# Performance work log

Measured on AMD Instinct MI355X. Metric: run time of the kernel, lower is better.

## Reference

```python
import jax, jax.numpy as jnp
import numpy as np

HID = 64
CTX = 64
STEPS = 2
RANK = 16
NODES = 1024
B, T = 16, 24
EPS = 1e-5


def _linear(x, W, b):
    # torch nn.Linear: x @ W.T + b, W is [out, in]
    return jnp.einsum('...i,oi->...o', x, W) + b


def _gelu(x):
    return jax.nn.gelu(x, approximate=False)


def _diffusion(adj, state, Ws, bs):
    # Ws: [S, out, in], bs: [S, out]
    term = jnp.zeros_like(state)
    for s in range(Ws.shape[0]):
        state = jnp.einsum('nm,btmf->btnf', adj, state)
        term = term + _linear(state, Ws[s], bs[s])
    return term


def setup_inputs() -> dict:
    key = jax.random.key(0)
    ks = jax.random.split(key, 32)
    f32 = jnp.float32
    def w(k, *shape, scale=None):
        s = scale if scale is not None else 1.0 / np.sqrt(shape[-1])
        return jax.random.uniform(k, shape, f32, -s, s)
    inp = {
        'x': jax.random.normal(ks[0], (B, T, NODES, HID), f32),
        'a_fwd': jax.random.uniform(ks[1], (NODES, NODES), f32),
        'context': jax.random.normal(ks[2], (B, T, NODES, CTX), f32),
        'W_self': w(ks[3], HID, HID), 'b_self': w(ks[4], HID),
        'W_fwd': w(ks[5], STEPS, HID, HID), 'b_fwd': w(ks[6], STEPS, HID),
        'W_bwd': w(ks[7], STEPS, HID, HID), 'b_bwd': w(ks[8], STEPS, HID),
        'W_adp': w(ks[9], STEPS, HID, HID), 'b_adp': w(ks[10], STEPS, HID),
        'Wg1': w(ks[11], HID, CTX), 'bg1': w(ks[12], HID),
        'Wg2': w(ks[13], 4, HID), 'bg2': w(ks[14], 4),
        'Ws1': w(ks[15], HID, CTX), 'bs1': w(ks[16], HID),
        'Ws2': w(ks[17], HID, HID), 'bs2': w(ks[18], HID),
        'W_src': w(ks[19], 1, CTX), 'b_src': w(ks[20], 1),
        'W_dst': w(ks[21], 1, CTX), 'b_dst': w(ks[22], 1),
        'emb_src': jax.random.normal(ks[23], (NODES, RANK), f32) * 0.02,
        'emb_dst': jax.random.normal(ks[24], (NODES, RANK), f32) * 0.02,
        'gamma': jnp.ones((HID,), f32), 'beta': jnp.zeros((HID,), f32),
    }
    return inp


def reference(x, a_fwd, context, W_self, b_self, W_fwd, b_fwd, W_bwd, b_bwd,
              W_adp, b_adp, Wg1, bg1, Wg2, bg2, Ws1, bs1, Ws2, bs2,
              W_src, b_src, W_dst, b_dst, emb_src, emb_dst, gamma, beta):
    a_bwd = a_fwd.T
    # adaptive adjacency: softmax(relu(Es @ Ed^T)) over last dim
    a_adp = jax.nn.softmax(jax.nn.relu(emb_src @ emb_dst.T), axis=-1)

    gates = jax.nn.sigmoid(_linear(_gelu(_linear(context, Wg1, bg1)), Wg2, bg2))  # [b,t,n,4]
    scale = jax.nn.sigmoid(_linear(_gelu(_linear(context, Ws1, bs1)), Ws2, bs2))  # [b,t,n,F]
    src_gate = jax.nn.sigmoid(_linear(context, W_src, b_src))  # [b,t,n,1]
    dst_gate = jax.nn.sigmoid(_linear(context, W_dst, b_dst))  # [b,t,n,1]

    self_term = _linear(x, W_self, b_self)
    fwd_term = _diffusion(a_fwd, x * dst_gate, W_fwd, b_fwd)
    bwd_term = _diffusion(a_bwd, x * src_gate, W_bwd, b_bwd)
    adp_term = _diffusion(a_adp, x, W_adp, b_adp)

    mixed = (gates[..., 0:1] * self_term + gates[..., 1:2] * fwd_term
             + gates[..., 2:3] * bwd_term + gates[..., 3:4] * adp_term) * scale

    h = x + _gelu(mixed)  # dropout is identity in eval mode
    mu = jnp.mean(h, axis=-1, keepdims=True)
    var = jnp.mean(jnp.square(h - mu), axis=-1, keepdims=True)
    return (h - mu) * jax.lax.rsqrt(var + EPS) * gamma + beta
```

## Files before the change

### kernel.cpp

```cpp
#include <hip/hip_runtime.h>
#include <math.h>

typedef unsigned short u16;
typedef short short8 __attribute__((ext_vector_type(8)));
typedef float f32x4 __attribute__((ext_vector_type(4)));

#define LN_EPS 1e-5f

__device__ __forceinline__ float gelu_exact(float x){
    return 0.5f * x * (1.0f + erff(x * 0.70710678118654752f));
}
__device__ __forceinline__ float sigmoidf_(float x){
    return 1.0f / (1.0f + __expf(-x));
}
__device__ __forceinline__ u16 f2bf(float f){
    unsigned u = __float_as_uint(f);
    u += 0x7fffu + ((u >> 16) & 1u);
    return (u16)(u >> 16);
}
__device__ __forceinline__ float b2f(u16 u){
    return __uint_as_float(((unsigned)u) << 16);
}

#define GLLDS(gp, lp) __builtin_amdgcn_global_load_lds( \
    (const __attribute__((address_space(1))) unsigned int*)(const void*)(gp), \
    (__attribute__((address_space(3))) unsigned int*)(void*)(lp), 16, 0, 0)

__global__ __launch_bounds__(256) void k_adp(const float* __restrict__ es,
                                             const float* __restrict__ ed,
                                             u16* __restrict__ aadp){
    __shared__ float srow[1024];
    __shared__ float s_es[16];
    __shared__ float sredm[4];
    __shared__ float sreds[4];
    const int n   = blockIdx.x;
    const int tid = threadIdx.x;
    const int wid = tid >> 6, lane = tid & 63;
    if (tid < 16) s_es[tid] = es[n*16 + tid];
    __syncthreads();
    float lmax = 0.0f;
    for (int m = tid; m < 1024; m += 256){
        const float* edm = ed + m*16;
        float z = 0.f;
        #pragma unroll
        for (int r = 0; r < 16; r++) z = fmaf(s_es[r], edm[r], z);
        z = fmaxf(z, 0.0f);
        srow[m] = z;
        lmax = fmaxf(lmax, z);
    }
    #pragma unroll
    for (int o = 32; o > 0; o >>= 1) lmax = fmaxf(lmax, __shfl_xor(lmax, o, 64));
    if (lane == 0) sredm[wid] = lmax;
    __syncthreads();
    const float tmax = fmaxf(fmaxf(sredm[0], sredm[1]), fmaxf(sredm[2], sredm[3]));
    float lsum = 0.f;
    for (int m = tid; m < 1024; m += 256){
        float e = expf(srow[m] - tmax);
        srow[m] = e;
        lsum += e;
    }
    #pragma unroll
    for (int o = 32; o > 0; o >>= 1) lsum += __shfl_xor(lsum, o, 64);
    if (lane == 0) sreds[wid] = lsum;
    __syncthreads();
    const float inv = 1.0f / (sreds[0] + sreds[1] + sreds[2] + sreds[3]);
    for (int m = tid; m < 1024; m += 256) aadp[(size_t)n*1024 + m] = f2bf(srow[m] * inv);
}

__global__ __launch_bounds__(256) void k_cvt(const float* __restrict__ in,
                                             u16* __restrict__ out){
    const int i = blockIdx.x*256 + threadIdx.x;
    const float4 v = ((const float4*)in)[i];
    ushort4 o;
    o.x = f2bf(v.x); o.y = f2bf(v.y); o.z = f2bf(v.z); o.w = f2bf(v.w);
    ((ushort4*)out)[i] = o;
}

__global__ __launch_bounds__(256) void k_bwd(const float* __restrict__ a,
                                             u16* __restrict__ at){
    __shared__ float t[32][33];
    const int bx = blockIdx.x*32, by = blockIdx.y*32;
    const int tx = threadIdx.x & 31, ty = threadIdx.x >> 5;
    #pragma unroll
    for (int i = 0; i < 4; i++)
        t[ty + 8*i][tx] = a[(size_t)(by + ty + 8*i)*1024 + bx + tx];
    __syncthreads();
    #pragma unroll
    for (int i = 0; i < 4; i++)
        at[(size_t)(bx + ty + 8*i)*1024 + by + tx] = f2bf(t[tx][ty + 8*i]);
}

__global__ __launch_bounds__(256, 2) void k_gating(
    const float* __restrict__ x,    const float* __restrict__ ctx,
    const float* __restrict__ Wg1,  const float* __restrict__ bg1,
    const float* __restrict__ Wg2,  const float* __restrict__ bg2,
    const float* __restrict__ Ws1,  const float* __restrict__ bs1,
    const float* __restrict__ Ws2,  const float* __restrict__ bs2,
    const float* __restrict__ Wsrc, const float* __restrict__ bsrc,
    const float* __restrict__ Wdst, const float* __restrict__ bdst,
    const float* __restrict__ Wself,const float* __restrict__ bself,
    float* __restrict__ gates, u16* __restrict__ scaleb,
    float* __restrict__ acc,
    u16* __restrict__ xTp, u16* __restrict__ xTd, u16* __restrict__ xTs)
{
    __shared__ u16 H1[16384];
    __shared__ u16 H2[16384];
    __shared__ float sgate[256], dgate[256];

    const int tid  = threadIdx.x;
    const int wv   = tid >> 6, lane = tid & 63;
    const int lr   = lane & 15, lg = lane >> 4;
    const int wtok = wv * 64;
    const int tokbase = blockIdx.x * 256;
    const int bt = blockIdx.x >> 2;
    const int n0 = (blockIdx.x & 3) * 256;

    auto stage_coop = [&](u16* H, const float* g){
        #pragma unroll
        for (int i = 0; i < 16; i++){
            const int fid = i*256 + tid;
            const int t = fid >> 4, q = fid & 15;
            const float4 v = *(const float4*)&g[(size_t)t*64 + q*4];
            ushort4 s;
            s.x = f2bf(v.x); s.y = f2bf(v.y); s.z = f2bf(v.z); s.w = f2bf(v.w);
            *(ushort4*)&H[t*64 + ((((q>>1) ^ (t & 7)) << 3) | ((q & 1)*4))] = s;
        }
    };
    auto afrag = [&](const u16* H, int row, int kb)->short8{
        return *(const short8*)&H[wv*4096 + row*64 + ((kb ^ (row & 7)) << 3)];
    };
    auto wfrag = [&](const float* W, int o, int kb8)->short8{
        const float4 a = *(const float4*)&W[o*64 + kb8];
        const float4 b = *(const float4*)&W[o*64 + kb8 + 4];
        short8 s;
        s[0]=f2bf(a.x); s[1]=f2bf(a.y); s[2]=f2bf(a.z); s[3]=f2bf(a.w);
        s[4]=f2bf(b.x); s[5]=f2bf(b.y); s[6]=f2bf(b.z); s[7]=f2bf(b.w);
        return s;
    };
    auto gemm64 = [&](const u16* Hs, const float* W, const float* bias, f32x4 (&c)[4][4]){
        #pragma unroll
        for (int n = 0; n < 4; n++){
            const float bv = bias[n*16 + lr];
            #pragma unroll
            for (int m = 0; m < 4; m++){ f32x4 t = {bv,bv,bv,bv}; c[m][n] = t; }
        }
        #pragma unroll
        for (int kk = 0; kk < 2; kk++){
            short8 a[4];
            #pragma unroll
            for (int m = 0; m < 4; m++) a[m] = afrag(Hs, m*16 + lr, kk*4 + lg);
            #pragma unroll
            for (int n = 0; n < 4; n++){
                const short8 w = wfrag(W, n*16 + lr, kk*32 + lg*8);
                #pragma unroll
                for (int m = 0; m < 4; m++)
                    c[m][n] = __builtin_amdgcn_mfma_f32_16x16x32_bf16(a[m], w, c[m][n], 0,0,0);
            }
        }
    };
    auto storeH = [&](u16* Hd, f32x4 (&c)[4][4]){
        #pragma unroll
        for (int m = 0; m < 4; m++)
            #pragma unroll
            for (int n = 0; n < 4; n++){
                const int f = n*16 + lr;
                #pragma unroll
                for (int r = 0; r < 4; r++){
                    const int t = m*16 + lg*4 + r;
                    Hd[wv*4096 + t*64 + ((((f>>3) ^ (t & 7)) << 3) | (f & 7))] = f2bf(c[m][n][r]);
                }
            }
    };

    stage_coop(H1, ctx + (size_t)tokbase*64);
    __syncthreads();

    f32x4 c[4][4];

    gemm64(H1, Wg1, bg1, c);
    #pragma unroll
    for (int m = 0; m < 4; m++)
        #pragma unroll
        for (int n = 0; n < 4; n++)
            #pragma unroll
            for (int r = 0; r < 4; r++) c[m][n][r] = gelu_exact(c[m][n][r]);
    storeH(H2, c);

    {
        f32x4 c2[4];
        const float bv = (lr == 0) ? bsrc[0] : (lr == 1 ? bdst[0] : 0.f);
        #pragma unroll
        for (int m = 0; m < 4; m++){ f32x4 t = {bv,bv,bv,bv}; c2[m] = t; }
        #pragma unroll
        for (int kk = 0; kk < 2; kk++){
            short8 a[4];
            #pragma unroll
            for (int m = 0; m < 4; m++) a[m] = afrag(H1, m*16 + lr, kk*4 + lg);
            short8 w = {0,0,0,0,0,0,0,0};
            if (lr == 0) w = wfrag(Wsrc, 0, kk*32 + lg*8);
            else if (lr == 1) w = wfrag(Wdst, 0, kk*32 + lg*8);
            #pragma unroll
            for (int m = 0; m < 4; m++)
                c2[m] = __builtin_amdgcn_mfma_f32_16x16x32_bf16(a[m], w, c2[m], 0,0,0);
        }
        #pragma unroll
        for (int m = 0; m < 4; m++)
            #pragma unroll
            for (int r = 0; r < 4; r++){
                const int t = wtok + m*16 + lg*4 + r;
                const float v = sigmoidf_(c2[m][r]);
                if (lr == 0) sgate[t] = v;
                if (lr == 1) dgate[t] = v;
            }
    }

    gemm64(H1, Ws1, bs1, c);
    #pragma unroll
    for (int m = 0; m < 4; m++)
        #pragma unroll
        for (int n = 0; n < 4; n++)
            #pragma unroll
            for (int r = 0; r < 4; r++) c[m][n][r] = gelu_exact(c[m][n][r]);
    storeH(H1, c);

    float g0[4][4];
    {
        f32x4 c3[4];
        const float bv = (lr < 4) ? bg2[lr] : 0.f;
        #pragma unroll
        for (int m = 0; m < 4; m++){ f32x4 t = {bv,bv,bv,bv}; c3[m] = t; }
        #pragma unroll
        for (int kk = 0; kk < 2; kk++){
            short8 a[4];
            #pragma unroll
            for (int m = 0; m < 4; m++) a[m] = afrag(H2, m*16 + lr, kk*4 + lg);
            short8 w = {0,0,0,0,0,0,0,0};
            if (lr < 4) w = wfrag(Wg2, lr, kk*32 + lg*8);
            #pragma unroll
            for (int m = 0; m < 4; m++)
                c3[m] = __builtin_amdgcn_mfma_f32_16x16x32_bf16(a[m], w, c3[m], 0,0,0);
        }
        #pragma unroll
        for (int m = 0; m < 4; m++)
            #pragma unroll
            for (int r = 0; r < 4; r++){
                const float v = sigmoidf_(c3[m][r]);
                if (lr < 4)
                    gates[(size_t)(tokbase + wtok + m*16 + lg*4 + r)*4 + lr] = v;
                g0[m][r] = __shfl(v, lane & 48, 64);
            }
    }

    gemm64(H1, Ws2, bs2, c);
    #pragma unroll
    for (int m = 0; m < 4; m++)
        #pragma unroll
        for (int n = 0; n < 4; n++)
            #pragma unroll
            for (int r = 0; r < 4; r++) c[m][n][r] = sigmoidf_(c[m][n][r]);
    storeH(H1, c);
    {
        #pragma unroll
        for (int it = 0; it < 8; it++){
            const int r2  = wtok + it*8 + (lane >> 3);
            const int sub = lane & 7;
            const short8 v = *(const short8*)&H1[r2*64 + ((sub ^ (r2 & 7)) << 3)];
            *(short8*)&scaleb[(size_t)(tokbase + r2)*64 + sub*8] = v;
        }
    }

    __syncthreads();
    stage_coop(H2, x + (size_t)tokbase*64);
    __syncthreads();

    gemm64(H2, Wself, bself, c);
    #pragma unroll
    for (int m = 0; m < 4; m++)
        #pragma unroll
        for (int n = 0; n < 4; n++)
            #pragma unroll
            for (int r = 0; r < 4; r++)
                acc[(size_t)(tokbase + wtok + m*16 + lg*4 + r)*64 + n*16 + lr]
                    = g0[m][r] * c[m][n][r];

    {
        const float dg = dgate[tid], sg = sgate[tid];
        const size_t ob = (size_t)bt*65536 + n0 + tid;
        #pragma unroll
        for (int fb = 0; fb < 8; fb++){
            const short8 v = *(const short8*)&H2[tid*64 + ((fb ^ (tid & 7)) << 3)];
            #pragma unroll
            for (int j = 0; j < 8; j++){
                const u16 raw = (u16)v[j];
                const float xv = b2f(raw);
                const size_t o = ob + (size_t)(fb*8 + j)*1024;
                xTp[o] = raw;
                xTd[o] = f2bf(xv * dg);
                xTs[o] = f2bf(xv * sg);
            }
        }
    }
}

template<bool WRITE_TMP>
__global__ __launch_bounds__(256, 2) void k_diffmm(
    const u16* __restrict__ adj,  const u16* __restrict__ srcT,
    const float* __restrict__ W,  const float* __restrict__ bias,
    const float* __restrict__ gates, const int branch,
    float* __restrict__ acc, u16* __restrict__ tmpT)
{
    __shared__ u16 sA[2][256*64];
    __shared__ u16 sB[2][64*64];

    const int tid = threadIdx.x;
    const int fb_ = blockIdx.x;
    const int s_  = (fb_ & 7) * 192 + (fb_ >> 3);
    const int bt  = s_ >> 2;
    const int n0  = (s_ & 3) * 256;
    const int wv  = tid >> 6, lane = tid & 63;
    const int lr  = lane & 15, lg = lane >> 4;
    const int wrow0 = wv * 64;

    const u16* asrc = adj  + (size_t)n0 * 1024;
    const u16* bsrc = srcT + (size_t)bt * 65536;

    auto stage = [&](int buf, int kt){
        const int m0 = kt * 64;
        #pragma unroll
        for (int i = 0; i < 8; i++){
            const int s = i*256 + tid;
            const int row = s >> 3, kbp = s & 7;
            const int kb = kbp ^ (row & 7);
            GLLDS(asrc + (size_t)row*1024 + m0 + kb*8, &sA[buf][s*8]);
        }
        #pragma unroll
        for (int i = 0; i < 2; i++){
            const int s = i*256 + tid;
            const int row = s >> 3, kbp = s & 7;
            const int kb = kbp ^ (row & 7);
            GLLDS(bsrc + (size_t)row*1024 + m0 + kb*8, &sB[buf][s*8]);
        }
    };

    const f32x4 z4 = {0.f, 0.f, 0.f, 0.f};
    f32x4 c[4][4];
    #pragma unroll
    for (int m = 0; m < 4; m++)
        #pragma unroll
        for (int n = 0; n < 4; n++) c[m][n] = z4;

    stage(0, 0);
    asm volatile("s_waitcnt vmcnt(0)" ::: "memory");
    __syncthreads();

    int cur = 0;
    for (int kt = 0; kt < 16; kt++){
        if (kt < 15) stage(cur ^ 1, kt + 1);
        const u16* A = sA[cur];
        const u16* B = sB[cur];
        short8 af[2][4], bfr[2][4];
        #pragma unroll
        for (int kk = 0; kk < 2; kk++){
            const int kb = lg + kk*4;
            #pragma unroll
            for (int m = 0; m < 4; m++){
                const int row = wrow0 + m*16 + lr;
                af[kk][m] = *(const short8*)&A[row*64 + ((kb ^ (row & 7)) << 3)];
            }
            #pragma unroll
            for (int n = 0; n < 4; n++){
                const int fr = n*16 + lr;
                bfr[kk][n] = *(const short8*)&B[fr*64 + ((kb ^ (fr & 7)) << 3)];
            }
        }
        #pragma unroll
        for (int kk = 0; kk < 2; kk++)
            #pragma unroll
            for (int m = 0; m < 4; m++)
                #pragma unroll
                for (int n = 0; n < 4; n++)
                    c[m][n] = __builtin_amdgcn_mfma_f32_16x16x32_bf16(
                        af[kk][m], bfr[kk][n], c[m][n], 0, 0, 0);
        asm volatile("s_waitcnt vmcnt(0)" ::: "memory");
        __syncthreads();
        cur ^= 1;
    }

    u16* yT = &sA[0][0];
    u16* sW = &sB[0][0];
    #pragma unroll
    for (int m = 0; m < 4; m++)
        #pragma unroll
        for (int n = 0; n < 4; n++){
            const int f = n*16 + lr;
            #pragma unroll
            for (int r = 0; r < 4; r++){
                const int row = wrow0 + m*16 + lg*4 + r;
                yT[row*64 + (((f >> 3) ^ (row & 7)) << 3) + (f & 7)] = f2bf(c[m][n][r]);
            }
        }
    for (int i = tid; i < 4096; i += 256){
        const int o = i >> 6, f = i & 63;
        sW[o*64 + (((f >> 3) ^ (o & 7)) << 3) + (f & 7)] = f2bf(W[i]);
    }
    __syncthreads();

    if (WRITE_TMP){
        const size_t ob = (size_t)bt*65536 + n0 + tid;
        #pragma unroll
        for (int fbk = 0; fbk < 8; fbk++){
            const short8 v = *(const short8*)&yT[tid*64 + ((fbk ^ (tid & 7)) << 3)];
            #pragma unroll
            for (int j = 0; j < 8; j++)
                tmpT[ob + (size_t)(fbk*8 + j)*1024] = (u16)v[j];
        }
    }

    f32x4 lin[4][4];
    #pragma unroll
    for (int m = 0; m < 4; m++)
        #pragma unroll
        for (int n = 0; n < 4; n++) lin[m][n] = z4;
    #pragma unroll
    for (int kk = 0; kk < 2; kk++){
        const int kb = lg + kk*4;
        short8 ya[4], wb[4];
        #pragma unroll
        for (int m = 0; m < 4; m++){
            const int row = wrow0 + m*16 + lr;
            ya[m] = *(const short8*)&yT[row*64 + ((kb ^ (row & 7)) << 3)];
        }
        #pragma unroll
        for (int n = 0; n < 4; n++){
            const int o = n*16 + lr;
            wb[n] = *(const short8*)&sW[o*64 + ((kb ^ (o & 7)) << 3)];
        }
        #pragma unroll
        for (int m = 0; m < 4; m++)
            #pragma unroll
            for (int n = 0; n < 4; n++)
                lin[m][n] = __builtin_amdgcn_mfma_f32_16x16x32_bf16(
                    ya[m], wb[n], lin[m][n], 0, 0, 0);
    }

    #pragma unroll
    for (int m = 0; m < 4; m++){
        float g[4];
        #pragma unroll
        for (int r = 0; r < 4; r++){
            const int node = n0 + wrow0 + m*16 + lg*4 + r;
            g[r] = gates[((size_t)bt*1024 + node)*4 + branch];
        }
        #pragma unroll
        for (int n = 0; n < 4; n++){
            const int f  = n*16 + lr;
            const float bv = bias[f];
            #pragma unroll
            for (int r = 0; r < 4; r++){
                const int node = n0 + wrow0 + m*16 + lg*4 + r;
                float* p = &acc[((size_t)bt*1024 + node)*64 + f];
                *p += g[r] * (lin[m][n][r] + bv);
            }
        }
    }
}

__global__ __launch_bounds__(256) void k_final(
    const float* __restrict__ x, const u16* __restrict__ scaleb,
    const float* __restrict__ gamma, const float* __restrict__ beta,
    float* __restrict__ out)
{
    const int tid = threadIdx.x;
    const int w = tid >> 6, lane = tid & 63;
    const size_t tok  = (size_t)blockIdx.x*4 + w;
    const size_t base = tok*64 + lane;
    const float mixed = out[base] * b2f(scaleb[base]);
    const float h = x[base] + gelu_exact(mixed);
    float mu = h;
    #pragma unroll
    for (int o = 32; o > 0; o >>= 1) mu += __shfl_xor(mu, o, 64);
    mu *= (1.0f/64.0f);
    const float d = h - mu;
    float v = d*d;
    #pragma unroll
    for (int o = 32; o > 0; o >>= 1) v += __shfl_xor(v, o, 64);
    v *= (1.0f/64.0f);
    out[base] = d * rsqrtf(v + LN_EPS) * gamma[lane] + beta[lane];
}

extern "C" void kernel_launch(void* const* d_in, const int* in_sizes, int n_in,
                              void* d_out, int out_size, void* d_ws, size_t ws_size,
                              hipStream_t stream)
{
    const float* x      = (const float*)d_in[0];
    const float* a_fwd  = (const float*)d_in[1];
    const float* ctx    = (const float*)d_in[2];
    const float* W_self = (const float*)d_in[3];
    const float* b_self = (const float*)d_in[4];
    const float* W_fwd  = (const float*)d_in[5];
    const float* b_fwd  = (const float*)d_in[6];
    const float* W_bwd  = (const float*)d_in[7];
    const float* b_bwd  = (const float*)d_in[8];
    const float* W_adp  = (const float*)d_in[9];
    const float* b_adp  = (const float*)d_in[10];
    const float* Wg1    = (const float*)d_in[11];
    const float* bg1    = (const float*)d_in[12];
    const float* Wg2    = (const float*)d_in[13];
    const float* bg2    = (const float*)d_in[14];
    const float* Ws1    = (const float*)d_in[15];
    const float* bs1    = (const float*)d_in[16];
    const float* Ws2    = (const float*)d_in[17];
    const float* bs2    = (const float*)d_in[18];
    const float* W_src  = (const float*)d_in[19];
    const float* b_src  = (const float*)d_in[20];
    const float* W_dst  = (const float*)d_in[21];
    const float* b_dst  = (const float*)d_in[22];
    const float* emb_src= (const float*)d_in[23];
    const float* emb_dst= (const float*)d_in[24];
    const float* gamma  = (const float*)d_in[25];
    const float* beta   = (const float*)d_in[26];

    float* out = (float*)d_out;
    char*  w   = (char*)d_ws;
    const size_t MB48 = 50331648ull;
    u16* afwd_bf = (u16*)(w);
    u16* abwd_bf = (u16*)(w + 2097152ull);
    u16* aadp_bf = (u16*)(w + 4194304ull);
    u16* xTp     = (u16*)(w + 6291456ull);
    u16* xTd     = (u16*)(w + 6291456ull + 1*MB48);
    u16* xTs     = (u16*)(w + 6291456ull + 2*MB48);
    u16* tmpT    = (u16*)(w + 6291456ull + 3*MB48);
    u16* scaleb  = (u16*)(w + 6291456ull + 4*MB48);
    float* gates = (float*)(w + 6291456ull + 5*MB48);

    k_adp   <<<1024, 256, 0, stream>>>(emb_src, emb_dst, aadp_bf);
    k_cvt   <<<1024, 256, 0, stream>>>(a_fwd, afwd_bf);
    k_bwd   <<<dim3(32,32), 256, 0, stream>>>(a_fwd, abwd_bf);
    k_gating<<<1536, 256, 0, stream>>>(x, ctx, Wg1,bg1, Wg2,bg2, Ws1,bs1, Ws2,bs2,
                                       W_src,b_src, W_dst,b_dst, W_self,b_self,
                                       gates, scaleb, out, xTp, xTd, xTs);

    k_diffmm<true ><<<1536,256,0,stream>>>(afwd_bf, xTd,  W_fwd,      b_fwd,    gates, 1, out, tmpT);
    k_diffmm<false><<<1536,256,0,stream>>>(afwd_bf, tmpT, W_fwd+4096, b_fwd+64, gates, 1, out, tmpT);
    k_diffmm<true ><<<1536,256,0,stream>>>(abwd_bf, xTs,  W_bwd,      b_bwd,    gates, 2, out, tmpT);
    k_diffmm<false><<<1536,256,0,stream>>>(abwd_bf, tmpT, W_bwd+4096, b_bwd+64, gates, 2, out, tmpT);
    k_diffmm<true ><<<1536,256,0,stream>>>(aadp_bf, xTp,  W_adp,      b_adp,    gates, 3, out, tmpT);
    k_diffmm<false><<<1536,256,0,stream>>>(aadp_bf, tmpT, W_adp+4096, b_adp+64, gates, 3, out, tmpT);

    k_final <<<98304, 256, 0, stream>>>(x, scaleb, gamma, beta, out);
}
```

Baseline: 1.055 ms.

## Fuse final LayerNorm into last diffusion GEMM, merge adjacency converts, shrink gating tiles

Folds the GELU, residual and LayerNorm epilogue into the last adaptive-diffusion GEMM kernel. This drops the separate k_final pass and its full re-read and re-write of the output. The fp32-to-bf16 conversion and the transposed conversion of the forward adjacency now run in one kernel, so a_fwd is read once. The gating kernel's tile is halved to 128 tokens with a launch bound of 4 blocks per SM, aiming for higher occupancy at the cost of more blocks and re-staged weights.

```diff
diff --git a/kernel.cpp b/kernel.cpp
--- a/kernel.cpp
+++ b/kernel.cpp
@@ -67,30 +67,25 @@
     for (int m = tid; m < 1024; m += 256) aadp[(size_t)n*1024 + m] = f2bf(srow[m] * inv);
 }
 
-__global__ __launch_bounds__(256) void k_cvt(const float* __restrict__ in,
-                                             u16* __restrict__ out){
-    const int i = blockIdx.x*256 + threadIdx.x;
-    const float4 v = ((const float4*)in)[i];
-    ushort4 o;
-    o.x = f2bf(v.x); o.y = f2bf(v.y); o.z = f2bf(v.z); o.w = f2bf(v.w);
-    ((ushort4*)out)[i] = o;
-}
-
-__global__ __launch_bounds__(256) void k_bwd(const float* __restrict__ a,
-                                             u16* __restrict__ at){
+__global__ __launch_bounds__(256) void k_cvtbwd(const float* __restrict__ a,
+                                                u16* __restrict__ afwd,
+                                                u16* __restrict__ abwd){
     __shared__ float t[32][33];
     const int bx = blockIdx.x*32, by = blockIdx.y*32;
     const int tx = threadIdx.x & 31, ty = threadIdx.x >> 5;
     #pragma unroll
+    for (int i = 0; i < 4; i++){
+        const float v = a[(size_t)(by + ty + 8*i)*1024 + bx + tx];
+        t[ty + 8*i][tx] = v;
+        afwd[(size_t)(by + ty + 8*i)*1024 + bx + tx] = f2bf(v);
+    }
+    __syncthreads();
+    #pragma unroll
     for (int i = 0; i < 4; i++)
-        t[ty + 8*i][tx] = a[(size_t)(by + ty + 8*i)*1024 + bx + tx];
-    __syncthreads();
-    #pragma unroll
-    for (int i = 0; i < 4; i++)
-        at[(size_t)(bx + ty + 8*i)*1024 + by + tx] = f2bf(t[tx][ty + 8*i]);
-}
-
-__global__ __launch_bounds__(256, 2) void k_gating(
+        abwd[(size_t)(bx + ty + 8*i)*1024 + by + tx] = f2bf(t[tx][ty + 8*i]);
+}
+
+__global__ __launch_bounds__(256, 4) void k_gating(
     const float* __restrict__ x,    const float* __restrict__ ctx,
     const float* __restrict__ Wg1,  const float* __restrict__ bg1,
     const float* __restrict__ Wg2,  const float* __restrict__ bg2,
@@ -103,21 +98,21 @@
     float* __restrict__ acc,
     u16* __restrict__ xTp, u16* __restrict__ xTd, u16* __restrict__ xTs)
 {
-    __shared__ u16 H1[16384];
-    __shared__ u16 H2[16384];
-    __shared__ float sgate[256], dgate[256];
+    __shared__ u16 H1[8192];
+    __shared__ u16 H2[8192];
+    __shared__ float sgate[128], dgate[128];
 
     const int tid  = threadIdx.x;
     const int wv   = tid >> 6, lane = tid & 63;
     const int lr   = lane & 15, lg = lane >> 4;
-    const int wtok = wv * 64;
-    const int tokbase = blockIdx.x * 256;
-    const int bt = blockIdx.x >> 2;
-    const int n0 = (blockIdx.x & 3) * 256;
+    const int wtok = wv * 32;
+    const int tokbase = blockIdx.x * 128;
+    const int bt = blockIdx.x >> 3;
+    const int n0 = (blockIdx.x & 7) * 128;
 
     auto stage_coop = [&](u16* H, const float* g){
         #pragma unroll
-        for (int i = 0; i < 16; i++){
+        for (int i = 0; i < 8; i++){
             const int fid = i*256 + tid;
             const int t = fid >> 4, q = fid & 15;
             const float4 v = *(const float4*)&g[(size_t)t*64 + q*4];
@@ -127,7 +122,7 @@
         }
     };
     auto afrag = [&](const u16* H, int row, int kb)->short8{
-        return *(const short8*)&H[wv*4096 + row*64 + ((kb ^ (row & 7)) << 3)];
+        return *(const short8*)&H[wv*2048 + row*64 + ((kb ^ (row & 7)) << 3)];
     };
     auto wfrag = [&](const float* W, int o, int kb8)->short8{
         const float4 a = *(const float4*)&W[o*64 + kb8];
@@ -137,37 +132,37 @@
         s[4]=f2bf(b.x); s[5]=f2bf(b.y); s[6]=f2bf(b.z); s[7]=f2bf(b.w);
         return s;
     };
-    auto gemm64 = [&](const u16* Hs, const float* W, const float* bias, f32x4 (&c)[4][4]){
+    auto gemm32 = [&](const u16* Hs, const float* W, const float* bias, f32x4 (&c)[2][4]){
         #pragma unroll
         for (int n = 0; n < 4; n++){
             const float bv = bias[n*16 + lr];
             #pragma unroll
-            for (int m = 0; m < 4; m++){ f32x4 t = {bv,bv,bv,bv}; c[m][n] = t; }
+            for (int m = 0; m < 2; m++){ f32x4 t = {bv,bv,bv,bv}; c[m][n] = t; }
         }
         #pragma unroll
         for (int kk = 0; kk < 2; kk++){
-            short8 a[4];
-            #pragma unroll
-            for (int m = 0; m < 4; m++) a[m] = afrag(Hs, m*16 + lr, kk*4 + lg);
+            short8 a[2];
+            #pragma unroll
+            for (int m = 0; m < 2; m++) a[m] = afrag(Hs, m*16 + lr, kk*4 + lg);
             #pragma unroll
             for (int n = 0; n < 4; n++){
                 const short8 w = wfrag(W, n*16 + lr, kk*32 + lg*8);
                 #pragma unroll
-                for (int m = 0; m < 4; m++)
+                for (int m = 0; m < 2; m++)
                     c[m][n] = __builtin_amdgcn_mfma_f32_16x16x32_bf16(a[m], w, c[m][n], 0,0,0);
             }
         }
     };
-    auto storeH = [&](u16* Hd, f32x4 (&c)[4][4]){
-        #pragma unroll
-        for (int m = 0; m < 4; m++)
+    auto storeH = [&](u16* Hd, f32x4 (&c)[2][4]){
+        #pragma unroll
+        for (int m = 0; m < 2; m++)
             #pragma unroll
             for (int n = 0; n < 4; n++){
                 const int f = n*16 + lr;
                 #pragma unroll
                 for (int r = 0; r < 4; r++){
                     const int t = m*16 + lg*4 + r;
-                    Hd[wv*4096 + t*64 + ((((f>>3) ^ (t & 7)) << 3) | (f & 7))] = f2bf(c[m][n][r]);
+                    Hd[wv*2048 + t*64 + ((((f>>3) ^ (t & 7)) << 3) | (f & 7))] = f2bf(c[m][n][r]);
                 }
             }
     };
@@ -175,11 +170,11 @@
     stage_coop(H1, ctx + (size_t)tokbase*64);
     __syncthreads();
 
-    f32x4 c[4][4];
-
-    gemm64(H1, Wg1, bg1, c);
-    #pragma unroll
-    for (int m = 0; m < 4; m++)
+    f32x4 c[2][4];
+
+    gemm32(H1, Wg1, bg1, c);
+    #pragma unroll
+    for (int m = 0; m < 2; m++)
         #pragma unroll
         for (int n = 0; n < 4; n++)
             #pragma unroll
@@ -187,24 +182,24 @@
     storeH(H2, c);
 
     {
-        f32x4 c2[4];
+        f32x4 c2[2];
         const float bv = (lr == 0) ? bsrc[0] : (lr == 1 ? bdst[0] : 0.f);
         #pragma unroll
-        for (int m = 0; m < 4; m++){ f32x4 t = {bv,bv,bv,bv}; c2[m] = t; }
+        for (int m = 0; m < 2; m++){ f32x4 t = {bv,bv,bv,bv}; c2[m] = t; }
         #pragma unroll
         for (int kk = 0; kk < 2; kk++){
-            short8 a[4];
-            #pragma unroll
-            for (int m = 0; m < 4; m++) a[m] = afrag(H1, m*16 + lr, kk*4 + lg);
+            short8 a[2];
+            #pragma unroll
+            for (int m = 0; m < 2; m++) a[m] = afrag(H1, m*16 + lr, kk*4 + lg);
             short8 w = {0,0,0,0,0,0,0,0};
             if (lr == 0) w = wfrag(Wsrc, 0, kk*32 + lg*8);
             else if (lr == 1) w = wfrag(Wdst, 0, kk*32 + lg*8);
             #pragma unroll
-            for (int m = 0; m < 4; m++)
+            for (int m = 0; m < 2; m++)
                 c2[m] = __builtin_amdgcn_mfma_f32_16x16x32_bf16(a[m], w, c2[m], 0,0,0);
         }
         #pragma unroll
-        for (int m = 0; m < 4; m++)
+        for (int m = 0; m < 2; m++)
             #pragma unroll
             for (int r = 0; r < 4; r++){
                 const int t = wtok + m*16 + lg*4 + r;
@@ -214,34 +209,34 @@
             }
     }
 
-    gemm64(H1, Ws1, bs1, c);
-    #pragma unroll
-    for (int m = 0; m < 4; m++)
+    gemm32(H1, Ws1, bs1, c);
+    #pragma unroll
+    for (int m = 0; m < 2; m++)
         #pragma unroll
         for (int n = 0; n < 4; n++)
             #pragma unroll
             for (int r = 0; r < 4; r++) c[m][n][r] = gelu_exact(c[m][n][r]);
     storeH(H1, c);
 
-    float g0[4][4];
+    float g0[2][4];
     {
-        f32x4 c3[4];
+        f32x4 c3[2];
         const float bv = (lr < 4) ? bg2[lr] : 0.f;
         #pragma unroll
-        for (int m = 0; m < 4; m++){ f32x4 t = {bv,bv,bv,bv}; c3[m] = t; }
+        for (int m = 0; m < 2; m++){ f32x4 t = {bv,bv,bv,bv}; c3[m] = t; }
         #pragma unroll
         for (int kk = 0; kk < 2; kk++){
-            short8 a[4];
-            #pragma unroll
-            for (int m = 0; m < 4; m++) a[m] = afrag(H2, m*16 + lr, kk*4 + lg);
+            short8 a[2];
+            #pragma unroll
+            for (int m = 0; m < 2; m++) a[m] = afrag(H2, m*16 + lr, kk*4 + lg);
             short8 w = {0,0,0,0,0,0,0,0};
             if (lr < 4) w = wfrag(Wg2, lr, kk*32 + lg*8);
             #pragma unroll
-            for (int m = 0; m < 4; m++)
+            for (int m = 0; m < 2; m++)
                 c3[m] = __builtin_amdgcn_mfma_f32_16x16x32_bf16(a[m], w, c3[m], 0,0,0);
         }
         #pragma unroll
-        for (int m = 0; m < 4; m++)
+        for (int m = 0; m < 2; m++)
             #pragma unroll
             for (int r = 0; r < 4; r++){
                 const float v = sigmoidf_(c3[m][r]);
@@ -251,9 +246,9 @@
             }
     }
 
-    gemm64(H1, Ws2, bs2, c);
-    #pragma unroll
-    for (int m = 0; m < 4; m++)
+    gemm32(H1, Ws2, bs2, c);
+    #pragma unroll
+    for (int m = 0; m < 2; m++)
         #pragma unroll
         for (int n = 0; n < 4; n++)
             #pragma unroll
@@ -261,7 +256,7 @@
     storeH(H1, c);
     {
         #pragma unroll
-        for (int it = 0; it < 8; it++){
+        for (int it = 0; it < 4; it++){
             const int r2  = wtok + it*8 + (lane >> 3);
             const int sub = lane & 7;
             const short8 v = *(const short8*)&H1[r2*64 + ((sub ^ (r2 & 7)) << 3)];
@@ -273,9 +268,9 @@
     stage_coop(H2, x + (size_t)tokbase*64);
     __syncthreads();
 
-    gemm64(H2, Wself, bself, c);
-    #pragma unroll
-    for (int m = 0; m < 4; m++)
+    gemm32(H2, Wself, bself, c);
+    #pragma unroll
+    for (int m = 0; m < 2; m++)
         #pragma unroll
         for (int n = 0; n < 4; n++)
             #pragma unroll
@@ -284,11 +279,14 @@
                     = g0[m][r] * c[m][n][r];
 
     {
-        const float dg = dgate[tid], sg = sgate[tid];
-        const size_t ob = (size_t)bt*65536 + n0 + tid;
-        #pragma unroll
-        for (int fb = 0; fb < 8; fb++){
-            const short8 v = *(const short8*)&H2[tid*64 + ((fb ^ (tid & 7)) << 3)];
+        const int tok  = tid & 127;
+        const int fbh  = tid >> 7;
+        const float dg = dgate[tok], sg = sgate[tok];
+        const size_t ob = (size_t)bt*65536 + n0 + tok;
+        #pragma unroll
+        for (int q = 0; q < 4; q++){
+            const int fb = fbh*4 + q;
+            const short8 v = *(const short8*)&H2[tok*64 + ((fb ^ (tok & 7)) << 3)];
             #pragma unroll
             for (int j = 0; j < 8; j++){
                 const u16 raw = (u16)v[j];
@@ -302,12 +300,14 @@
     }
 }
 
-template<bool WRITE_TMP>
+template<bool WRITE_TMP, bool FINAL>
 __global__ __launch_bounds__(256, 2) void k_diffmm(
     const u16* __restrict__ adj,  const u16* __restrict__ srcT,
     const float* __restrict__ W,  const float* __restrict__ bias,
     const float* __restrict__ gates, const int branch,
-    float* __restrict__ acc, u16* __restrict__ tmpT)
+    float* __restrict__ acc, u16* __restrict__ tmpT,
+    const float* __restrict__ x, const u16* __restrict__ scaleb,
+    const float* __restrict__ gamma, const float* __restrict__ beta)
 {
     __shared__ u16 sA[2][256*64];
     __shared__ u16 sB[2][64*64];
@@ -443,49 +443,61 @@
                     ya[m], wb[n], lin[m][n], 0, 0, 0);
     }
 
-    #pragma unroll
-    for (int m = 0; m < 4; m++){
-        float g[4];
-        #pragma unroll
-        for (int r = 0; r < 4; r++){
-            const int node = n0 + wrow0 + m*16 + lg*4 + r;
-            g[r] = gates[((size_t)bt*1024 + node)*4 + branch];
-        }
-        #pragma unroll
-        for (int n = 0; n < 4; n++){
-            const int f  = n*16 + lr;
-            const float bv = bias[f];
+    if constexpr (!FINAL){
+        #pragma unroll
+        for (int m = 0; m < 4; m++){
+            float g[4];
             #pragma unroll
             for (int r = 0; r < 4; r++){
                 const int node = n0 + wrow0 + m*16 + lg*4 + r;
-                float* p = &acc[((size_t)bt*1024 + node)*64 + f];
-                *p += g[r] * (lin[m][n][r] + bv);
-            }
-        }
-    }
-}
-
-__global__ __launch_bounds__(256) void k_final(
-    const float* __restrict__ x, const u16* __restrict__ scaleb,
-    const float* __restrict__ gamma, const float* __restrict__ beta,
-    float* __restrict__ out)
-{
-    const int tid = threadIdx.x;
-    const int w = tid >> 6, lane = tid & 63;
-    const size_t tok  = (size_t)blockIdx.x*4 + w;
-    const size_t base = tok*64 + lane;
-    const float mixed = out[base] * b2f(scaleb[base]);
-    const float h = x[base] + gelu_exact(mixed);
-    float mu = h;
-    #pragma unroll
-    for (int o = 32; o > 0; o >>= 1) mu += __shfl_xor(mu, o, 64);
-    mu *= (1.0f/64.0f);
-    const float d = h - mu;
-    float v = d*d;
-    #pragma unroll
-    for (int o = 32; o > 0; o >>= 1) v += __shfl_xor(v, o, 64);
-    v *= (1.0f/64.0f);
-    out[base] = d * rsqrtf(v + LN_EPS) * gamma[lane] + beta[lane];
+                g[r] = gates[((size_t)bt*1024 + node)*4 + branch];
+            }
+            #pragma unroll
+            for (int n = 0; n < 4; n++){
+                const int f  = n*16 + lr;
+                const float bv = bias[f];
+                #pragma unroll
+                for (int r = 0; r < 4; r++){
+                    const int node = n0 + wrow0 + m*16 + lg*4 + r;
+                    float* p = &acc[((size_t)bt*1024 + node)*64 + f];
+                    *p += g[r] * (lin[m][n][r] + bv);
+                }
+            }
+        }
+    } else {
+        #pragma unroll
+        for (int m = 0; m < 4; m++){
+            #pragma unroll
+            for (int r = 0; r < 4; r++){
+                const int node = n0 + wrow0 + m*16 + lg*4 + r;
+                const size_t tok = (size_t)bt*1024 + node;
+                const float g = gates[tok*4 + branch];
+                float h[4];
+                #pragma unroll
+                for (int n = 0; n < 4; n++){
+                    const int f = n*16 + lr;
+                    const float a = acc[tok*64 + f] + g * (lin[m][n][r] + bias[f]);
+                    const float mixed = a * b2f(scaleb[tok*64 + f]);
+                    h[n] = x[tok*64 + f] + gelu_exact(mixed);
+                }
+                float s = h[0] + h[1] + h[2] + h[3];
+                #pragma unroll
+                for (int o = 8; o > 0; o >>= 1) s += __shfl_xor(s, o, 64);
+                const float mu = s * (1.0f/64.0f);
+                float vs = 0.f;
+                #pragma unroll
+                for (int n = 0; n < 4; n++){ const float d = h[n] - mu; vs += d*d; }
+                #pragma unroll
+                for (int o = 8; o > 0; o >>= 1) vs += __shfl_xor(vs, o, 64);
+                const float inv = rsqrtf(vs * (1.0f/64.0f) + LN_EPS);
+                #pragma unroll
+                for (int n = 0; n < 4; n++){
+                    const int f = n*16 + lr;
+                    acc[tok*64 + f] = (h[n] - mu) * inv * gamma[f] + beta[f];
+                }
+            }
+        }
+    }
 }
 
 extern "C" void kernel_launch(void* const* d_in, const int* in_sizes, int n_in,
@@ -534,18 +546,27 @@
     float* gates = (float*)(w + 6291456ull + 5*MB48);
 
     k_adp   <<<1024, 256, 0, stream>>>(emb_src, emb_dst, aadp_bf);
-    k_cvt   <<<1024, 256, 0, stream>>>(a_fwd, afwd_bf);
-    k_bwd   <<<dim3(32,32), 256, 0, stream>>>(a_fwd, abwd_bf);
-    k_gating<<<1536, 256, 0, stream>>>(x, ctx, Wg1,bg1, Wg2,bg2, Ws1,bs1, Ws2,bs2,
+    k_cvtbwd<<<dim3(32,32), 256, 0, stream>>>(a_fwd, afwd_bf, abwd_bf);
+    k_gating<<<3072, 256, 0, stream>>>(x, ctx, Wg1,bg1, Wg2,bg2, Ws1,bs1, Ws2,bs2,
                                        W_src,b_src, W_dst,b_dst, W_self,b_self,
                                        gates, scaleb, out, xTp, xTd, xTs);
 
-    k_diffmm<true ><<<1536,256,0,stream>>>(afwd_bf, xTd,  W_fwd,      b_fwd,    gates, 1, out, tmpT);
-    k_diffmm<false><<<1536,256,0,stream>>>(afwd_bf, tmpT, W_fwd+4096, b_fwd+64, gates, 1, out, tmpT);
-    k_diffmm<true ><<<1536,256,0,stream>>>(abwd_bf, xTs,  W_bwd,      b_bwd,    gates, 2, out, tmpT);
-    k_diffmm<false><<<1536,256,0,stream>>>(abwd_bf, tmpT, W_bwd+4096, b_bwd+64, gates, 2, out, tmpT);
-    k_diffmm<true ><<<1536,256,0,stream>>>(aadp_bf, xTp,  W_adp,      b_adp,    gates, 3, out, tmpT);
-    k_diffmm<false><<<1536,256,0,stream>>>(aadp_bf, tmpT, W_adp+4096, b_adp+64, gates, 3, out, tmpT);
-
-    k_final <<<98304, 256, 0, stream>>>(x, scaleb, gamma, beta, out);
-}
+    k_diffmm<true ,false><<<1536,256,0,stream>>>(afwd_bf, xTd,  W_fwd,      b_fwd,
+                                                 gates, 1, out, tmpT,
+                                                 nullptr, nullptr, nullptr, nullptr);
+    k_diffmm<false,false><<<1536,256,0,stream>>>(afwd_bf, tmpT, W_fwd+4096, b_fwd+64,
+                                                 gates, 1, out, nullptr,
+                                                 nullptr, nullptr, nullptr, nullptr);
+    k_diffmm<true ,false><<<1536,256,0,stream>>>(abwd_bf, xTs,  W_bwd,      b_bwd,
+                                                 gates, 2, out, tmpT,
+                                                 nullptr, nullptr, nullptr, nullptr);
+    k_diffmm<false,false><<<1536,256,0,stream>>>(abwd_bf, tmpT, W_bwd+4096, b_bwd+64,
+                                                 gates, 2, out, nullptr,
+                                                 nullptr, nullptr, nullptr, nullptr);
+    k_diffmm<true ,false><<<1536,256,0,stream>>>(aadp_bf, xTp,  W_adp,      b_adp,
+                                                 gates, 3, out, tmpT,
+                                                 nullptr, nullptr, nullptr, nullptr);
+    k_diffmm<false,true ><<<1536,256,0,stream>>>(aadp_bf, tmpT, W_adp+4096, b_adp+64,
+                                                 gates, 3, out, nullptr,
+                                                 x, scaleb, gamma, beta);
+}
```

Result: no change. 1.053 ms (-0.2%).
